# Kernel tuning notes

Hardware: AMD Instinct MI355X
Metric: run time of the kernel (lower is better)

The kernel has to match this reference:

```python
import jax, jax.numpy as jnp
import numpy as np

L = 3
NUM_NODES = 4000
NUM_RELS = 200
V = 20
EMB = 128
HID = 128
OUT = 100
N = 50000
E = 800000
B = 32
DECAY = 0.03


def setup_inputs() -> dict:
    key = jax.random.key(0)
    ks = jax.random.split(key, 20)
    s = 0.05  # weight scale
    inp = {
        'node_emb': jax.random.normal(ks[0], (NUM_NODES, EMB), jnp.float32) * s,
        'rel_emb': jax.random.normal(ks[1], (NUM_RELS, EMB), jnp.float32) * s,
        'lin_w': jax.random.normal(ks[2], (HID, EMB), jnp.float32) * s,  # torch Linear weight [out,in]
        'lin_b': jnp.zeros((HID,), jnp.float32),
        'alpha_w': jax.random.normal(ks[3], (L, NUM_NODES, NUM_NODES), jnp.float32) * 0.01,
        'alpha_b': jnp.zeros((L, NUM_NODES), jnp.float32),
        'beta_w': jax.random.normal(ks[4], (L, NUM_NODES), jnp.float32) * 0.01,
        'beta_b': jnp.zeros((L,), jnp.float32),
        'wr_w': jax.random.normal(ks[5], (L, HID), jnp.float32) * s,
        'wr_b': jnp.zeros((L,), jnp.float32),
        'conv_w': jax.random.normal(ks[6], (L, HID, HID), jnp.float32) * s,
        'conv_b': jnp.zeros((L, HID), jnp.float32),
        'mlp_w': jax.random.normal(ks[7], (OUT, 2 * HID), jnp.float32) * s,
        'mlp_b': jnp.zeros((OUT,), jnp.float32),
        'visit_node': jax.random.uniform(ks[8], (B, V, NUM_NODES), jnp.float32),
        'ehr_nodes': jax.random.uniform(ks[9], (B, NUM_NODES), jnp.float32),
        'node_ids': jax.random.randint(ks[10], (N,), 0, NUM_NODES, jnp.int32),
        'rel_ids': jax.random.randint(ks[11], (E,), 0, NUM_RELS, jnp.int32),
        'edge_index': jax.random.randint(ks[12], (2, E), 0, N, jnp.int32),
        'batch': jnp.sort(jax.random.randint(ks[13], (N,), 0, B, jnp.int32)),
    }
    return inp


def reference(node_emb, rel_emb, lin_w, lin_b, alpha_w, alpha_b, beta_w, beta_b,
              wr_w, wr_b, conv_w, conv_b, mlp_w, mlp_b, visit_node, ehr_nodes,
              node_ids, rel_ids, edge_index, batch):
    # initial node / edge features
    x = node_emb[node_ids] @ lin_w.T + lin_b                # [N, HID]
    edge_attr = rel_emb[rel_ids] @ lin_w.T + lin_b          # [E, HID]

    # temporal decay per visit: lambda_j = exp(decay*(V - j)), shape [1, V, 1]
    j = jnp.arange(V, dtype=jnp.float32)
    lam = jnp.exp(DECAY * (V - j))[None, :, None]

    src = edge_index[0]
    dst = edge_index[1]
    xj_nid = node_ids[src]                                  # [E]
    xj_bat = batch[src]                                     # [E]

    for l in range(L):
        # alpha: softmax over the visit axis (dim=1)
        alpha = jax.nn.softmax(
            jnp.einsum('bvn,mn->bvm', visit_node, alpha_w[l]) + alpha_b[l], axis=1)
        beta = jnp.tanh(
            jnp.einsum('bvn,n->bv', visit_node, beta_w[l])[:, :, None] + beta_b[l]) * lam
        attn = jnp.sum(alpha * beta, axis=1)                # [B, NUM_NODES]
        e_attn = attn[xj_bat, xj_nid][:, None]              # [E, 1]

        # BiAttentionGNNConv message + add-aggregate
        w_rel = edge_attr @ wr_w[l][:, None] + wr_b[l]      # [E, 1]
        msg = jax.nn.relu(x[src] * e_attn + w_rel * edge_attr)
        agg = jax.ops.segment_sum(msg, dst, num_segments=N)
        out = agg + x                                       # eps = 0 -> (1+eps)=1
        x = out @ conv_w[l].T + conv_b[l]                   # conv.nn Linear
        x = jax.nn.relu(x)                                  # outer F.relu (dropout inactive in eval)

    # global mean pool over graphs
    cnt = jax.ops.segment_sum(jnp.ones((N,), x.dtype), batch, num_segments=B)
    x_graph = jax.ops.segment_sum(x, batch, num_segments=B) / jnp.maximum(cnt, 1.0)[:, None]

    # patient node embedding branch
    x_node = (ehr_nodes @ node_emb) / jnp.sum(ehr_nodes, axis=1, keepdims=True)
    x_node = x_node @ lin_w.T + lin_b                       # [B, HID]

    logits = jnp.concatenate([x_graph, x_node], axis=1) @ mlp_w.T + mlp_b
    return logits
```

## Files before the change

kernel.cpp:

```cpp
#include <hip/hip_runtime.h>
#include <hip/hip_bf16.h>
#include <stdint.h>

#define LL      3
#define NNODES  4000
#define NRELS   200
#define VV      20
#define EMB     128
#define HIDD    128
#define OUTD    100
#define WS_N    50000
#define WS_E    800000
#define BV      32
#define DECAYF  0.03f
#define AK      4032
#define ZSTRIDE ((long)LL*640*4000)
#define SCAN_NB 196
#define NPP     391

typedef __bf16 bf16x8 __attribute__((ext_vector_type(8)));
typedef __bf16 bf16x4 __attribute__((ext_vector_type(4)));
typedef __bf16 bf16x2 __attribute__((ext_vector_type(2)));
typedef float  f32x4  __attribute__((ext_vector_type(4)));

__device__ __forceinline__ void glds16(const __bf16* g, __bf16* l) {
    __builtin_amdgcn_global_load_lds((const __attribute__((address_space(1))) void*)g,
                                     (__attribute__((address_space(3))) void*)l, 16, 0, 0);
}

__global__ __launch_bounds__(256) void k_cvt2(const float* __restrict__ visit,
                                              const float* __restrict__ alpha_w,
                                              const float* __restrict__ beta_w,
                                              const float* __restrict__ beta_b,
                                              __bf16* __restrict__ visit_bf,
                                              __bf16* __restrict__ alpha_bf,
                                              float* __restrict__ betab) {
    long bid = blockIdx.x;
    const bool isv = bid < BV*VV;
    const float* ip; __bf16* op;
    if (isv) { ip = visit + bid*4000; op = visit_bf + bid*AK; }
    else     { long r = bid - BV*VV; ip = alpha_w + r*4000; op = alpha_bf + r*AK; }
    int t = threadIdx.x;
    float p0 = 0.f, p1 = 0.f, p2 = 0.f;
    if (t < 250) {
        const float4* p4 = (const float4*)ip + t*4;
        float4 f0 = p4[0], f1 = p4[1], f2 = p4[2], f3 = p4[3];
        bf16x8 h0, h1;
        h0[0]=(__bf16)f0.x; h0[1]=(__bf16)f0.y; h0[2]=(__bf16)f0.z; h0[3]=(__bf16)f0.w;
        h0[4]=(__bf16)f1.x; h0[5]=(__bf16)f1.y; h0[6]=(__bf16)f1.z; h0[7]=(__bf16)f1.w;
        h1[0]=(__bf16)f2.x; h1[1]=(__bf16)f2.y; h1[2]=(__bf16)f2.z; h1[3]=(__bf16)f2.w;
        h1[4]=(__bf16)f3.x; h1[5]=(__bf16)f3.y; h1[6]=(__bf16)f3.z; h1[7]=(__bf16)f3.w;
        ((bf16x8*)op)[t*2]   = h0;
        ((bf16x8*)op)[t*2+1] = h1;
        if (isv) {
            #pragma unroll
            for (int l = 0; l < LL; l++) {
                const float4* bw = (const float4*)(beta_w + (long)l*4000) + t*4;
                float4 b0 = bw[0], b1 = bw[1], b2 = bw[2], b3 = bw[3];
                float s = f0.x*b0.x + f0.y*b0.y + f0.z*b0.z + f0.w*b0.w
                        + f1.x*b1.x + f1.y*b1.y + f1.z*b1.z + f1.w*b1.w
                        + f2.x*b2.x + f2.y*b2.y + f2.z*b2.z + f2.w*b2.w
                        + f3.x*b3.x + f3.y*b3.y + f3.z*b3.z + f3.w*b3.w;
                if (l == 0) p0 = s; else if (l == 1) p1 = s; else p2 = s;
            }
        }
    } else if (t < 254) {
        bf16x8 zz;
        #pragma unroll
        for (int j = 0; j < 8; j++) zz[j] = (__bf16)0.f;
        ((bf16x8*)op)[500 + (t - 250)] = zz;
    }
    if (isv) {
        __shared__ float r0[256], r1[256], r2[256];
        r0[t] = p0; r1[t] = p1; r2[t] = p2;
        __syncthreads();
        for (int o = 128; o > 0; o >>= 1) {
            if (t < o) { r0[t] += r0[t+o]; r1[t] += r1[t+o]; r2[t] += r2[t+o]; }
            __syncthreads();
        }
        if (t == 0) {
            int v = (int)(bid % VV);
            float lam = __expf(DECAYF * (float)(VV - v));
            betab[0*BV*VV + bid] = tanhf(r0[0] + beta_b[0]) * lam;
            betab[1*BV*VV + bid] = tanhf(r1[0] + beta_b[1]) * lam;
            betab[2*BV*VV + bid] = tanhf(r2[0] + beta_b[2]) * lam;
        }
    }
}

__global__ __launch_bounds__(256)
void gemm_alpha(const __bf16* __restrict__ visit_bf, const __bf16* __restrict__ alpha_bf,
                __bf16* __restrict__ zpart)
{
    __shared__ __bf16 Ah[128*64];
    __shared__ __bf16 Bh[128*64];

    const int id   = blockIdx.x;
    const int xcd  = id & 7;
    const int slot = id >> 3;
    const int mi   = slot % 5;
    const int gix  = slot / 5;
    const int g    = xcd * 48 + gix;
    const int ni   = g & 31;
    const int lkh  = g >> 5;
    const int l    = lkh >> 2;
    const int kh   = lkh & 3;

    const __bf16* Ag = visit_bf;
    const __bf16* Bg = alpha_bf + (long)l * NNODES * AK;
    __bf16*       Cg = zpart + (long)kh * ZSTRIDE + (long)l * 640 * 4000;
    const int m0 = mi * 128;
    const int n0 = ni * 128;
    const int k0 = kh * 1024;
    const int k1 = (kh == 3) ? AK : (k0 + 1024);

    const int tid = threadIdx.x;
    const int wv  = tid >> 6;
    const int ln  = tid & 63;
    const int srow = ln >> 3;
    const int gsl  = (ln & 7) ^ srow;

    const __bf16* aA = Ag + (long)(m0 + wv*8 + srow) * AK + gsl*8;
    const __bf16* bB[4];
    #pragma unroll
    for (int t = 0; t < 4; t++) {
        int br = n0 + wv*8 + srow + t*32;
        if (br > NNODES-1) br = NNODES-1;
        bB[t] = Bg + (long)br * AK + gsl*8;
    }

    const int wm = (wv & 1) * 64;
    const int wn = (wv >> 1) * 64;
    const int lr = ln & 15;
    const int kq = ln >> 4;
    const int sw0 = lr & 7;

    f32x4 acc[4][4];
    #pragma unroll
    for (int i = 0; i < 4; i++)
        #pragma unroll
        for (int j = 0; j < 4; j++)
            acc[i][j] = (f32x4){0.f, 0.f, 0.f, 0.f};

    for (int kb = k0; kb < k1; kb += 64) {
        #pragma unroll
        for (int t = 0; t < 4; t++) {
            glds16(aA + (long)t*32*AK + kb, &Ah[(t*4 + wv) * 512]);
            glds16(bB[t] + kb,              &Bh[(t*4 + wv) * 512]);
        }
        __syncthreads();
        #pragma unroll
        for (int ks = 0; ks < 2; ks++) {
            const int sg = ((ks*4 + kq) ^ sw0) * 8;
            bf16x8 af[4], bfr[4];
            #pragma unroll
            for (int i = 0; i < 4; i++) {
                af[i]  = *(const bf16x8*)&Ah[(wm + i*16 + lr)*64 + sg];
                bfr[i] = *(const bf16x8*)&Bh[(wn + i*16 + lr)*64 + sg];
            }
            #pragma unroll
            for (int i = 0; i < 4; i++)
                #pragma unroll
                for (int j = 0; j < 4; j++)
                    acc[i][j] = __builtin_amdgcn_mfma_f32_16x16x32_bf16(af[i], bfr[j], acc[i][j], 0, 0, 0);
        }
        __syncthreads();
    }

    #pragma unroll
    for (int i = 0; i < 4; i++) {
        const int row_b = m0 + wm + i*16 + kq*4;
        #pragma unroll
        for (int j = 0; j < 4; j++) {
            const int col = n0 + wn + j*16 + lr;
            if (col < NNODES) {
                #pragma unroll
                for (int r = 0; r < 4; r++)
                    Cg[(long)(row_b + r)*4000 + col] = (__bf16)acc[i][j][r];
            }
        }
    }
}

#define BM 128
#define BN 128
#define BKG 32
#define LSTR 40

template<int SPLIT>
__device__ __forceinline__ void stage_tile(const float* __restrict__ G, int rows, int Kdim,
                                           int r0, int kb, int k1, __bf16* Sh, __bf16* Sl, int tid)
{
    const int sr  = tid >> 1;
    const int skc = (tid & 1) * 16;
    const int gr  = r0 + sr;
    const int gk  = kb + skc;
    float va[16];
    if (gr < rows && gk + 16 <= k1) {
        const float4* p4 = (const float4*)(G + (long)gr * Kdim + gk);
        #pragma unroll
        for (int q = 0; q < 4; q++) {
            float4 f = p4[q];
            va[4*q+0] = f.x; va[4*q+1] = f.y; va[4*q+2] = f.z; va[4*q+3] = f.w;
        }
    } else {
        #pragma unroll
        for (int j = 0; j < 16; j++) {
            int kk = gk + j;
            va[j] = (gr < rows && kk < k1) ? G[(long)gr * Kdim + kk] : 0.0f;
        }
    }
    bf16x8 h[2], lo[2];
    #pragma unroll
    for (int half = 0; half < 2; half++) {
        #pragma unroll
        for (int j = 0; j < 8; j++) {
            float v = va[half*8 + j];
            __bf16 hi = (__bf16)v;
            h[half][j]  = hi;
            lo[half][j] = (__bf16)(v - (float)hi);
        }
    }
    *(bf16x8*)&Sh[sr*LSTR + skc]     = h[0];
    *(bf16x8*)&Sh[sr*LSTR + skc + 8] = h[1];
    if (SPLIT) {
        *(bf16x8*)&Sl[sr*LSTR + skc]     = lo[0];
        *(bf16x8*)&Sl[sr*LSTR + skc + 8] = lo[1];
    }
}

template<int SPLIT, int RELU, int BIAS, int WRITEB>
__global__ __launch_bounds__(256)
void gemm_bt(const float* __restrict__ Ag, const float* __restrict__ Bg,
             float* __restrict__ Cg, const float* __restrict__ bias,
             __bf16* __restrict__ Xb, int M, int N, int K)
{
    __shared__ __bf16 Ah[BM*LSTR];
    __shared__ __bf16 Bh[BN*LSTR];
    __shared__ __bf16 Alo[SPLIT ? BM*LSTR : 1];
    __shared__ __bf16 Blo[SPLIT ? BN*LSTR : 1];

    const int tid = threadIdx.x;
    const int m0 = blockIdx.x * BM;
    const int n0 = blockIdx.y * BN;

    const int wave = tid >> 6;
    const int lane = tid & 63;
    const int wm = (wave & 1) * 64;
    const int wn = (wave >> 1) * 64;
    const int lr = lane & 15;
    const int kq = lane >> 4;

    f32x4 acc[4][4];
    #pragma unroll
    for (int i = 0; i < 4; i++)
        #pragma unroll
        for (int j = 0; j < 4; j++)
            acc[i][j] = (f32x4){0.f, 0.f, 0.f, 0.f};

    for (int kb = 0; kb < K; kb += BKG) {
        stage_tile<SPLIT>(Ag, M, K, m0, kb, K, Ah, Alo, tid);
        stage_tile<SPLIT>(Bg, N, K, n0, kb, K, Bh, Blo, tid);
        __syncthreads();

        bf16x8 af[4], bfr[4];
        #pragma unroll
        for (int i = 0; i < 4; i++) {
            af[i]  = *(const bf16x8*)&Ah[(wm + i*16 + lr)*LSTR + kq*8];
            bfr[i] = *(const bf16x8*)&Bh[(wn + i*16 + lr)*LSTR + kq*8];
        }
        #pragma unroll
        for (int i = 0; i < 4; i++)
            #pragma unroll
            for (int j = 0; j < 4; j++)
                acc[i][j] = __builtin_amdgcn_mfma_f32_16x16x32_bf16(af[i], bfr[j], acc[i][j], 0, 0, 0);

        if (SPLIT) {
            bf16x8 al[4], bl[4];
            #pragma unroll
            for (int i = 0; i < 4; i++) {
                al[i] = *(const bf16x8*)&Alo[(wm + i*16 + lr)*LSTR + kq*8];
                bl[i] = *(const bf16x8*)&Blo[(wn + i*16 + lr)*LSTR + kq*8];
            }
            #pragma unroll
            for (int i = 0; i < 4; i++)
                #pragma unroll
                for (int j = 0; j < 4; j++) {
                    acc[i][j] = __builtin_amdgcn_mfma_f32_16x16x32_bf16(af[i], bl[j], acc[i][j], 0, 0, 0);
                    acc[i][j] = __builtin_amdgcn_mfma_f32_16x16x32_bf16(al[i], bfr[j], acc[i][j], 0, 0, 0);
                }
        }
        __syncthreads();
    }

    #pragma unroll
    for (int i = 0; i < 4; i++) {
        const int row_b = m0 + wm + i*16 + kq*4;
        #pragma unroll
        for (int j = 0; j < 4; j++) {
            const int col = n0 + wn + j*16 + lr;
            if (col < N) {
                #pragma unroll
                for (int r = 0; r < 4; r++) {
                    const int row = row_b + r;
                    if (row < M) {
                        float v = acc[i][j][r];
                        if (BIAS) v += bias[col];
                        if (RELU) v = fmaxf(v, 0.0f);
                        Cg[(long)row*N + col] = v;
                        if (WRITEB) Xb[(long)row*N + col] = (__bf16)v;
                    }
                }
            }
        }
    }
}

__global__ void k_count(const int* __restrict__ dst, int* __restrict__ deg) {
    int e = blockIdx.x*256 + threadIdx.x;
    if (e < WS_E) atomicAdd(&deg[dst[e]], 1);
}

__global__ __launch_bounds__(256) void k_scan1(const int* __restrict__ deg, int* __restrict__ bsum) {
    __shared__ int red[256];
    int t = threadIdx.x;
    int i = blockIdx.x*256 + t;
    red[t] = (i < WS_N) ? deg[i] : 0;
    __syncthreads();
    for (int o = 128; o > 0; o >>= 1) {
        if (t < o) red[t] += red[t + o];
        __syncthreads();
    }
    if (t == 0) bsum[blockIdx.x] = red[0];
}

__global__ __launch_bounds__(256) void k_scan3(const int* __restrict__ deg, const int* __restrict__ bsum,
                                               int* __restrict__ offs, int* __restrict__ cursor) {
    __shared__ int sb[256];
    __shared__ int s[256];
    int t = threadIdx.x;
    int bv = (t < SCAN_NB) ? bsum[t] : 0;
    sb[t] = bv;
    __syncthreads();
    for (int o = 1; o < 256; o <<= 1) {
        int add = (t >= o) ? sb[t - o] : 0;
        __syncthreads();
        sb[t] += add;
        __syncthreads();
    }
    int base = (blockIdx.x == 0) ? 0 : sb[blockIdx.x - 1];

    int i = blockIdx.x*256 + t;
    int v = (i < WS_N) ? deg[i] : 0;
    s[t] = v;
    __syncthreads();
    for (int o = 1; o < 256; o <<= 1) {
        int add = (t >= o) ? s[t - o] : 0;
        __syncthreads();
        s[t] += add;
        __syncthreads();
    }
    if (i < WS_N) {
        int e = base + s[t] - v;
        offs[i] = e;
        cursor[i] = e;
    }
    if (blockIdx.x == 0 && t == 0) offs[WS_N] = WS_E;
}

__global__ void k_fill(const int* __restrict__ dst, const int* __restrict__ src,
                       const int* __restrict__ rel, int* __restrict__ cursor,
                       int2* __restrict__ sr) {
    int e = blockIdx.x*256 + threadIdx.x;
    if (e < WS_E) {
        int d = dst[e];
        int p = atomicAdd(&cursor[d], 1);
        sr[p] = make_int2(src[e], rel[e]);
    }
}

__global__ __launch_bounds__(128) void k_relfused(const float* __restrict__ rel_emb,
                                                  const float* __restrict__ lin_w,
                                                  const float* __restrict__ lin_b,
                                                  const float* __restrict__ wr_w,
                                                  const float* __restrict__ wr_b,
                                                  __bf16* __restrict__ relmsg) {
    int r = blockIdx.x;
    int o = threadIdx.x;
    __shared__ float row[128];
    __shared__ float red[128];
    row[o] = rel_emb[(long)r*EMB + o];
    __syncthreads();
    float wv = lin_b[o];
    #pragma unroll 4
    for (int k = 0; k < EMB; k++) wv += row[k] * lin_w[(long)o*EMB + k];
    #pragma unroll
    for (int l = 0; l < LL; l++) {
        red[o] = wv * wr_w[l*HIDD + o];
        __syncthreads();
        for (int s2 = 64; s2 > 0; s2 >>= 1) {
            if (o < s2) red[o] += red[o + s2];
            __syncthreads();
        }
        float wrel = red[0] + wr_b[l];
        __syncthreads();
        relmsg[((long)l*NRELS + r)*HIDD + o] = (__bf16)(wrel * wv);
    }
}

__global__ void k_xinit(const float* __restrict__ Wnode, const int* __restrict__ nid,
                        const int* __restrict__ batch, const float* __restrict__ attn,
                        float* __restrict__ x, __bf16* __restrict__ xb, float* __restrict__ an) {
    int t = blockIdx.x*256 + threadIdx.x;
    if (t >= WS_N*32) return;
    int i = t >> 5;
    int d = t & 31;
    int n = nid[i];
    float4 v = ((const float4*)Wnode)[n*32 + d];
    ((float4*)x)[i*32 + d] = v;
    bf16x4 b;
    b[0] = (__bf16)v.x; b[1] = (__bf16)v.y; b[2] = (__bf16)v.z; b[3] = (__bf16)v.w;
    ((bf16x4*)xb)[i*32 + d] = b;
    if (d < LL) an[(long)d*WS_N + i] = attn[((long)d*BV + batch[i]) * NNODES + n];
}

__global__ __launch_bounds__(256) void k_attnpool(const __bf16* __restrict__ zpart,
                                                  const float* __restrict__ beta, float* __restrict__ attn) {
    int m = blockIdx.x*256 + threadIdx.x;
    int b = blockIdx.y;
    int l = blockIdx.z;
    if (m >= NNODES) return;
    const __bf16* zp = zpart + ((long)l*640 + b*VV) * 4000 + m;
    const float* bet = beta + (l*BV + b) * VV;
    float zv[VV];
    float mx = -1e30f;
    #pragma unroll
    for (int v = 0; v < VV; v++) {
        long o = (long)v * 4000;
        float s = (float)zp[o] + (float)zp[ZSTRIDE + o] + (float)zp[2*ZSTRIDE + o] + (float)zp[3*ZSTRIDE + o];
        zv[v] = s;
        mx = fmaxf(mx, s);
    }
    float s = 0.f, ws = 0.f;
    #pragma unroll
    for (int v = 0; v < VV; v++) {
        float e = __expf(zv[v] - mx);
        s += e;
        ws += e * bet[v];
    }
    attn[((long)l*BV + b) * NNODES + m] = ws / s;
}

__global__ __launch_bounds__(256) void k_agg(const float* __restrict__ x, const __bf16* __restrict__ xb,
                                             const float* __restrict__ an,
                                             const __bf16* __restrict__ relmsg_l, const int* __restrict__ offs,
                                             const int2* __restrict__ sr,
                                             float* __restrict__ outb) {
    int node = blockIdx.x*4 + (threadIdx.x >> 6);
    if (node >= WS_N) return;
    int lane = threadIdx.x & 63;
    int half = lane >> 5;
    int lh   = lane & 31;
    int e0 = offs[node], e1 = offs[node + 1];
    const bf16x4* xb4 = (const bf16x4*)xb;
    const bf16x4* rm4 = (const bf16x4*)relmsg_l;
    float a0 = 0.f, a1 = 0.f, a2 = 0.f, a3 = 0.f;
    int e = e0;
    for (; e + 8 <= e1; e += 8) {
        int2 pe[4];
        #pragma unroll
        for (int q = 0; q < 4; q++) pe[q] = sr[e + 2*q + half];
        float aq[4]; bf16x4 gv[4], mv[4];
        #pragma unroll
        for (int q = 0; q < 4; q++) aq[q] = an[pe[q].x];
        #pragma unroll
        for (int q = 0; q < 4; q++) gv[q] = xb4[pe[q].x*32 + lh];
        #pragma unroll
        for (int q = 0; q < 4; q++) mv[q] = rm4[pe[q].y*32 + lh];
        #pragma unroll
        for (int q = 0; q < 4; q++) {
            a0 += fmaxf((float)gv[q][0]*aq[q] + (float)mv[q][0], 0.f);
            a1 += fmaxf((float)gv[q][1]*aq[q] + (float)mv[q][1], 0.f);
            a2 += fmaxf((float)gv[q][2]*aq[q] + (float)mv[q][2], 0.f);
            a3 += fmaxf((float)gv[q][3]*aq[q] + (float)mv[q][3], 0.f);
        }
    }
    for (; e < e1; e += 2) {
        int ei = e + half;
        bool vld = ei < e1;
        int2 pe = sr[vld ? ei : e];
        float aa = vld ? an[pe.x] : 0.f;
        bf16x4 ga = xb4[pe.x*32 + lh];
        bf16x4 va = rm4[pe.y*32 + lh];
        float vm = vld ? 1.f : 0.f;
        a0 += vm * fmaxf((float)ga[0]*aa + (float)va[0], 0.f);
        a1 += vm * fmaxf((float)ga[1]*aa + (float)va[1], 0.f);
        a2 += vm * fmaxf((float)ga[2]*aa + (float)va[2], 0.f);
        a3 += vm * fmaxf((float)ga[3]*aa + (float)va[3], 0.f);
    }
    a0 += __shfl_xor(a0, 32);
    a1 += __shfl_xor(a1, 32);
    a2 += __shfl_xor(a2, 32);
    a3 += __shfl_xor(a3, 32);
    if (half == 0) {
        float4 xo = ((const float4*)x)[node*32 + lh];
        float4 r;
        r.x = a0 + xo.x; r.y = a1 + xo.y; r.z = a2 + xo.z; r.w = a3 + xo.w;
        ((float4*)outb)[node*32 + lh] = r;
    }
}

__global__ __launch_bounds__(256) void k_pool(const float* __restrict__ x,
                                              const int* __restrict__ batch,
                                              const float* __restrict__ ehr,
                                              const float* __restrict__ node_emb,
                                              float* __restrict__ xgsum,
                                              float* __restrict__ xnsum,
                                              float* __restrict__ esum) {
    if (blockIdx.x < NPP) {
        int r0 = blockIdx.x * 128;
        int d = threadIdx.x & 127;
        int rofs = threadIdx.x >> 7;
        int r1 = min(r0 + 128, WS_N);
        float acc = 0.f;
        int curb = -1;
        for (int i = r0 + rofs; i < r1; i += 2) {
            int b = batch[i];
            if (b != curb) {
                if (curb >= 0) atomicAdd(&xgsum[curb*HIDD + d], acc);
                acc = 0.f; curb = b;
            }
            acc += x[(long)i*HIDD + d];
        }
        if (curb >= 0) atomicAdd(&xgsum[curb*HIDD + d], acc);
    } else {
        int id = blockIdx.x - NPP;
        int b = id >> 4;
        int c = id & 15;
        int d = threadIdx.x;
        int n0 = c * (NNODES/16), n1 = n0 + (NNODES/16);
        __shared__ float red[256];
        if (d < 128) {
            float acc = 0.f;
            for (int n = n0; n < n1; n++)
                acc += ehr[b*NNODES + n] * node_emb[(long)n*HIDD + d];
            atomicAdd(&xnsum[b*HIDD + d], acc);
        }
        float s = 0.f;
        for (int n = n0 + d; n < n1; n += 256) s += ehr[b*NNODES + n];
        red[d] = s; __syncthreads();
        for (int o = 128; o > 0; o >>= 1) {
            if (d < o) red[d] += red[d + o];
            __syncthreads();
        }
        if (d == 0) atomicAdd(&esum[b], red[0]);
    }
}

__global__ __launch_bounds__(128) void k_head(const float* __restrict__ xgsum,
                                              const float* __restrict__ xnsum,
                                              const float* __restrict__ esum,
                                              const int* __restrict__ batch,
                                              const float* __restrict__ lin_w, const float* __restrict__ lin_b,
                                              const float* __restrict__ mlp_w, const float* __restrict__ mlp_b,
                                              float* __restrict__ out) {
    int b = blockIdx.x;
    int d = threadIdx.x;
    int lo = 0, hi = WS_N;
    while (lo < hi) { int mid = (lo + hi) >> 1; if (batch[mid] < b) lo = mid + 1; else hi = mid; }
    int s0 = lo;
    lo = 0; hi = WS_N;
    while (lo < hi) { int mid = (lo + hi) >> 1; if (batch[mid] < b + 1) lo = mid + 1; else hi = mid; }
    int cnt = max(lo - s0, 1);
    __shared__ float t1[128];
    __shared__ float cat[2*HIDD];
    t1[d]  = xnsum[b*HIDD + d] / esum[b];
    cat[d] = xgsum[b*HIDD + d] / (float)cnt;
    __syncthreads();
    float o2 = lin_b[d];
    for (int k2 = 0; k2 < HIDD; k2++) o2 += t1[k2] * lin_w[d*HIDD + k2];
    cat[HIDD + d] = o2;
    __syncthreads();
    if (d < OUTD) {
        float a = mlp_b[d];
        for (int j = 0; j < 2*HIDD; j++) a += cat[j] * mlp_w[d*2*HIDD + j];
        out[b*OUTD + d] = a;
    }
}

extern "C" void kernel_launch(void* const* d_in, const int* in_sizes, int n_in,
                              void* d_out, int out_size, void* d_ws, size_t ws_size,
                              hipStream_t stream)
{
    const float* node_emb = (const float*)d_in[0];
    const float* rel_emb  = (const float*)d_in[1];
    const float* lin_w    = (const float*)d_in[2];
    const float* lin_b    = (const float*)d_in[3];
    const float* alpha_w  = (const float*)d_in[4];
    const float* beta_w   = (const float*)d_in[6];
    const float* beta_b   = (const float*)d_in[7];
    const float* wr_w     = (const float*)d_in[8];
    const float* wr_b     = (const float*)d_in[9];
    const float* conv_w   = (const float*)d_in[10];
    const float* conv_b   = (const float*)d_in[11];
    const float* mlp_w    = (const float*)d_in[12];
    const float* mlp_b    = (const float*)d_in[13];
    const float* visit    = (const float*)d_in[14];
    const float* ehr      = (const float*)d_in[15];
    const int* node_ids   = (const int*)d_in[16];
    const int* rel_ids    = (const int*)d_in[17];
    const int* ei         = (const int*)d_in[18];
    const int* batch      = (const int*)d_in[19];
    const int* esrc = ei;
    const int* edst = ei + WS_E;
    float* out = (float*)d_out;

    char* p = (char*)d_ws;
    auto take = [&](size_t bytes) -> char* {
        char* q = p;
        p += (bytes + 255) & ~(size_t)255;
        return q;
    };
    __bf16* zpart    = (__bf16*)take((size_t)4*ZSTRIDE*2);
    __bf16* visit_bf = (__bf16*)take((size_t)(BV*VV)*AK*2);
    char*   big      = take((size_t)LL*NNODES*AK*2);
    float* betab  = (float*)take((size_t)LL*BV*VV*4);
    float* xgsum  = (float*)take((size_t)BV*HIDD*4);
    float* xnsum  = (float*)take((size_t)BV*HIDD*4);
    float* esum   = (float*)take((size_t)BV*4);
    int* deg      = (int*)take((size_t)WS_N*4);
    size_t zero_bytes = (size_t)((char*)(deg + WS_N) - (char*)xgsum);
    int* offs     = (int*)take((size_t)(WS_N+1)*4);
    int* cursor   = (int*)take((size_t)WS_N*4);
    int* bsum     = (int*)take((size_t)SCAN_NB*4);
    if ((size_t)(p - (char*)d_ws) > ws_size) return;

    __bf16* alpha_bf = (__bf16*)big;
    char* q = big;
    auto carve = [&](size_t bytes) -> char* {
        char* r = q;
        q += (bytes + 255) & ~(size_t)255;
        return r;
    };
    float*  x      = (float*)carve((size_t)WS_N*HIDD*4);
    __bf16* xb     = (__bf16*)carve((size_t)WS_N*HIDD*2);
    int2*   sr     = (int2*)carve((size_t)WS_E*8);
    float*  attn   = (float*)carve((size_t)LL*BV*NNODES*4);
    float*  attnnd = (float*)carve((size_t)LL*WS_N*4);
    float*  Wnode  = (float*)carve((size_t)NNODES*HIDD*4);
    __bf16* relmsg = (__bf16*)carve((size_t)LL*NRELS*HIDD*2);
    float*  aggbuf = (float*)zpart;

    (void)hipMemsetAsync(xgsum, 0, zero_bytes, stream);

    k_cvt2<<<dim3(BV*VV + LL*NNODES), 256, 0, stream>>>(visit, alpha_w, beta_w, beta_b,
                                                        visit_bf, alpha_bf, betab);
    gemm_alpha<<<dim3(1920), 256, 0, stream>>>(visit_bf, alpha_bf, zpart);
    k_attnpool<<<dim3((NNODES+255)/256, BV, LL), 256, 0, stream>>>(zpart, betab, attn);

    k_count<<<dim3((WS_E+255)/256), 256, 0, stream>>>(edst, deg);
    k_scan1<<<dim3(SCAN_NB), 256, 0, stream>>>(deg, bsum);
    k_scan3<<<dim3(SCAN_NB), 256, 0, stream>>>(deg, bsum, offs, cursor);
    k_fill<<<dim3((WS_E+255)/256), 256, 0, stream>>>(edst, esrc, rel_ids, cursor, sr);

    gemm_bt<1,0,1,0><<<dim3((NNODES+BM-1)/BM, 1, 1), 256, 0, stream>>>(
        node_emb, lin_w, Wnode, lin_b, nullptr, NNODES, HIDD, HIDD);
    k_relfused<<<dim3(NRELS), 128, 0, stream>>>(rel_emb, lin_w, lin_b, wr_w, wr_b, relmsg);
    k_xinit<<<dim3((WS_N*32+255)/256), 256, 0, stream>>>(Wnode, node_ids, batch, attn, x, xb, attnnd);

    for (int l = 0; l < LL; l++) {
        k_agg<<<dim3((WS_N+3)/4), 256, 0, stream>>>(
            x, xb, attnnd + (size_t)l*WS_N, relmsg + (size_t)l*NRELS*HIDD, offs, sr, aggbuf);
        gemm_bt<1,1,1,1><<<dim3((WS_N+BM-1)/BM, 1, 1), 256, 0, stream>>>(
            aggbuf, conv_w + (size_t)l*HIDD*HIDD, x, conv_b + (size_t)l*HIDD, xb,
            WS_N, HIDD, HIDD);
    }

    k_pool<<<dim3(NPP + 16*BV), 256, 0, stream>>>(x, batch, ehr, node_emb, xgsum, xnsum, esum);
    k_head<<<BV, 128, 0, stream>>>(xgsum, xnsum, esum, batch, lin_w, lin_b, mlp_w, mlp_b, out);
}
```

Before: 820.1 us.

## Pack edge src/rel into 32-bit, widen agg loads, fuse degree count

Edge records are packed into one uint32 (16-bit src, 16-bit rel) instead of int2, which halves CSR edge traffic in the fill and aggregation kernels. k_agg now uses 16 lanes with bf16x8 loads per edge and processes 4 edges in parallel per wavefront, reduced with two shuffles. The degree-count kernel is folded into the conversion kernel's grid to save a launch, and the last layer's GEMM skips writing the bf16 copy of x. Packing src into 16 bits relies on node indices staying below 65536 (N=50000 fits), and the grid-size change drops the node bound check, which is only safe because N is divisible by 4.

```diff
diff --git a/kernel.cpp b/kernel.cpp
--- a/kernel.cpp
+++ b/kernel.cpp
@@ -17,6 +17,8 @@
 #define ZSTRIDE ((long)LL*640*4000)
 #define SCAN_NB 196
 #define NPP     391
+#define CVT_NB  (BV*VV + LL*NNODES)
+#define CNT_NB  ((WS_E+255)/256)
 
 typedef __bf16 bf16x8 __attribute__((ext_vector_type(8)));
 typedef __bf16 bf16x4 __attribute__((ext_vector_type(4)));
@@ -34,13 +36,20 @@
                                               const float* __restrict__ beta_b,
                                               __bf16* __restrict__ visit_bf,
                                               __bf16* __restrict__ alpha_bf,
-                                              float* __restrict__ betab) {
+                                              float* __restrict__ betab,
+                                              const int* __restrict__ edst,
+                                              int* __restrict__ deg) {
     long bid = blockIdx.x;
+    int t = threadIdx.x;
+    if (bid >= CVT_NB) {
+        int e = (int)(bid - CVT_NB)*256 + t;
+        if (e < WS_E) atomicAdd(&deg[edst[e]], 1);
+        return;
+    }
     const bool isv = bid < BV*VV;
     const float* ip; __bf16* op;
     if (isv) { ip = visit + bid*4000; op = visit_bf + bid*AK; }
     else     { long r = bid - BV*VV; ip = alpha_w + r*4000; op = alpha_bf + r*AK; }
-    int t = threadIdx.x;
     float p0 = 0.f, p1 = 0.f, p2 = 0.f;
     if (t < 250) {
         const float4* p4 = (const float4*)ip + t*4;
@@ -316,11 +325,6 @@
     }
 }
 
-__global__ void k_count(const int* __restrict__ dst, int* __restrict__ deg) {
-    int e = blockIdx.x*256 + threadIdx.x;
-    if (e < WS_E) atomicAdd(&deg[dst[e]], 1);
-}
-
 __global__ __launch_bounds__(256) void k_scan1(const int* __restrict__ deg, int* __restrict__ bsum) {
     __shared__ int red[256];
     int t = threadIdx.x;
@@ -370,12 +374,12 @@
 
 __global__ void k_fill(const int* __restrict__ dst, const int* __restrict__ src,
                        const int* __restrict__ rel, int* __restrict__ cursor,
-                       int2* __restrict__ sr) {
+                       uint32_t* __restrict__ sr) {
     int e = blockIdx.x*256 + threadIdx.x;
     if (e < WS_E) {
         int d = dst[e];
         int p = atomicAdd(&cursor[d], 1);
-        sr[p] = make_int2(src[e], rel[e]);
+        sr[p] = (uint32_t)src[e] | ((uint32_t)rel[e] << 16);
     }
 }
 
@@ -454,59 +458,65 @@
 __global__ __launch_bounds__(256) void k_agg(const float* __restrict__ x, const __bf16* __restrict__ xb,
                                              const float* __restrict__ an,
                                              const __bf16* __restrict__ relmsg_l, const int* __restrict__ offs,
-                                             const int2* __restrict__ sr,
+                                             const uint32_t* __restrict__ sr,
                                              float* __restrict__ outb) {
     int node = blockIdx.x*4 + (threadIdx.x >> 6);
-    if (node >= WS_N) return;
     int lane = threadIdx.x & 63;
-    int half = lane >> 5;
-    int lh   = lane & 31;
+    int eh = lane >> 4;
+    int lh = lane & 15;
     int e0 = offs[node], e1 = offs[node + 1];
-    const bf16x4* xb4 = (const bf16x4*)xb;
-    const bf16x4* rm4 = (const bf16x4*)relmsg_l;
-    float a0 = 0.f, a1 = 0.f, a2 = 0.f, a3 = 0.f;
+    const bf16x8* xb8 = (const bf16x8*)xb;
+    const bf16x8* rm8 = (const bf16x8*)relmsg_l;
+    float acc[8];
+    #pragma unroll
+    for (int d = 0; d < 8; d++) acc[d] = 0.f;
     int e = e0;
     for (; e + 8 <= e1; e += 8) {
-        int2 pe[4];
-        #pragma unroll
-        for (int q = 0; q < 4; q++) pe[q] = sr[e + 2*q + half];
-        float aq[4]; bf16x4 gv[4], mv[4];
-        #pragma unroll
-        for (int q = 0; q < 4; q++) aq[q] = an[pe[q].x];
-        #pragma unroll
-        for (int q = 0; q < 4; q++) gv[q] = xb4[pe[q].x*32 + lh];
-        #pragma unroll
-        for (int q = 0; q < 4; q++) mv[q] = rm4[pe[q].y*32 + lh];
-        #pragma unroll
-        for (int q = 0; q < 4; q++) {
-            a0 += fmaxf((float)gv[q][0]*aq[q] + (float)mv[q][0], 0.f);
-            a1 += fmaxf((float)gv[q][1]*aq[q] + (float)mv[q][1], 0.f);
-            a2 += fmaxf((float)gv[q][2]*aq[q] + (float)mv[q][2], 0.f);
-            a3 += fmaxf((float)gv[q][3]*aq[q] + (float)mv[q][3], 0.f);
-        }
-    }
-    for (; e < e1; e += 2) {
-        int ei = e + half;
-        bool vld = ei < e1;
-        int2 pe = sr[vld ? ei : e];
-        float aa = vld ? an[pe.x] : 0.f;
-        bf16x4 ga = xb4[pe.x*32 + lh];
-        bf16x4 va = rm4[pe.y*32 + lh];
-        float vm = vld ? 1.f : 0.f;
-        a0 += vm * fmaxf((float)ga[0]*aa + (float)va[0], 0.f);
-        a1 += vm * fmaxf((float)ga[1]*aa + (float)va[1], 0.f);
-        a2 += vm * fmaxf((float)ga[2]*aa + (float)va[2], 0.f);
-        a3 += vm * fmaxf((float)ga[3]*aa + (float)va[3], 0.f);
-    }
-    a0 += __shfl_xor(a0, 32);
-    a1 += __shfl_xor(a1, 32);
-    a2 += __shfl_xor(a2, 32);
-    a3 += __shfl_xor(a3, 32);
-    if (half == 0) {
-        float4 xo = ((const float4*)x)[node*32 + lh];
-        float4 r;
-        r.x = a0 + xo.x; r.y = a1 + xo.y; r.z = a2 + xo.z; r.w = a3 + xo.w;
-        ((float4*)outb)[node*32 + lh] = r;
+        uint32_t p0 = sr[e + eh], p1 = sr[e + 4 + eh];
+        int s0 = p0 & 0xFFFF, r0 = p0 >> 16;
+        int s1 = p1 & 0xFFFF, r1 = p1 >> 16;
+        float a0 = an[s0], a1 = an[s1];
+        bf16x8 g0 = xb8[s0*16 + lh], g1 = xb8[s1*16 + lh];
+        bf16x8 m0 = rm8[r0*16 + lh], m1 = rm8[r1*16 + lh];
+        #pragma unroll
+        for (int d = 0; d < 8; d++) {
+            acc[d] += fmaxf((float)g0[d]*a0 + (float)m0[d], 0.f);
+            acc[d] += fmaxf((float)g1[d]*a1 + (float)m1[d], 0.f);
+        }
+    }
+    for (; e + 4 <= e1; e += 4) {
+        uint32_t p = sr[e + eh];
+        int s = p & 0xFFFF, r = p >> 16;
+        float a = an[s];
+        bf16x8 g = xb8[s*16 + lh];
+        bf16x8 m = rm8[r*16 + lh];
+        #pragma unroll
+        for (int d = 0; d < 8; d++)
+            acc[d] += fmaxf((float)g[d]*a + (float)m[d], 0.f);
+    }
+    if (e + eh < e1) {
+        uint32_t p = sr[e + eh];
+        int s = p & 0xFFFF, r = p >> 16;
+        float a = an[s];
+        bf16x8 g = xb8[s*16 + lh];
+        bf16x8 m = rm8[r*16 + lh];
+        #pragma unroll
+        for (int d = 0; d < 8; d++)
+            acc[d] += fmaxf((float)g[d]*a + (float)m[d], 0.f);
+    }
+    #pragma unroll
+    for (int d = 0; d < 8; d++) {
+        acc[d] += __shfl_xor(acc[d], 16);
+        acc[d] += __shfl_xor(acc[d], 32);
+    }
+    if (eh == 0) {
+        float4 x0 = ((const float4*)x)[node*32 + lh*2];
+        float4 x1 = ((const float4*)x)[node*32 + lh*2 + 1];
+        float4 o0, o1;
+        o0.x = acc[0] + x0.x; o0.y = acc[1] + x0.y; o0.z = acc[2] + x0.z; o0.w = acc[3] + x0.w;
+        o1.x = acc[4] + x1.x; o1.y = acc[5] + x1.y; o1.z = acc[6] + x1.z; o1.w = acc[7] + x1.w;
+        ((float4*)outb)[node*32 + lh*2]     = o0;
+        ((float4*)outb)[node*32 + lh*2 + 1] = o1;
     }
 }
 
@@ -642,23 +652,22 @@
         q += (bytes + 255) & ~(size_t)255;
         return r;
     };
-    float*  x      = (float*)carve((size_t)WS_N*HIDD*4);
-    __bf16* xb     = (__bf16*)carve((size_t)WS_N*HIDD*2);
-    int2*   sr     = (int2*)carve((size_t)WS_E*8);
-    float*  attn   = (float*)carve((size_t)LL*BV*NNODES*4);
-    float*  attnnd = (float*)carve((size_t)LL*WS_N*4);
-    float*  Wnode  = (float*)carve((size_t)NNODES*HIDD*4);
-    __bf16* relmsg = (__bf16*)carve((size_t)LL*NRELS*HIDD*2);
-    float*  aggbuf = (float*)zpart;
+    float*    x      = (float*)carve((size_t)WS_N*HIDD*4);
+    __bf16*   xb     = (__bf16*)carve((size_t)WS_N*HIDD*2);
+    uint32_t* sr     = (uint32_t*)carve((size_t)WS_E*4);
+    float*    attn   = (float*)carve((size_t)LL*BV*NNODES*4);
+    float*    attnnd = (float*)carve((size_t)LL*WS_N*4);
+    float*    Wnode  = (float*)carve((size_t)NNODES*HIDD*4);
+    __bf16*   relmsg = (__bf16*)carve((size_t)LL*NRELS*HIDD*2);
+    float*    aggbuf = (float*)zpart;
 
     (void)hipMemsetAsync(xgsum, 0, zero_bytes, stream);
 
-    k_cvt2<<<dim3(BV*VV + LL*NNODES), 256, 0, stream>>>(visit, alpha_w, beta_w, beta_b,
-                                                        visit_bf, alpha_bf, betab);
+    k_cvt2<<<dim3(CVT_NB + CNT_NB), 256, 0, stream>>>(visit, alpha_w, beta_w, beta_b,
+                                                      visit_bf, alpha_bf, betab, edst, deg);
     gemm_alpha<<<dim3(1920), 256, 0, stream>>>(visit_bf, alpha_bf, zpart);
     k_attnpool<<<dim3((NNODES+255)/256, BV, LL), 256, 0, stream>>>(zpart, betab, attn);
 
-    k_count<<<dim3((WS_E+255)/256), 256, 0, stream>>>(edst, deg);
     k_scan1<<<dim3(SCAN_NB), 256, 0, stream>>>(deg, bsum);
     k_scan3<<<dim3(SCAN_NB), 256, 0, stream>>>(deg, bsum, offs, cursor);
     k_fill<<<dim3((WS_E+255)/256), 256, 0, stream>>>(edst, esrc, rel_ids, cursor, sr);
@@ -669,11 +678,16 @@
     k_xinit<<<dim3((WS_N*32+255)/256), 256, 0, stream>>>(Wnode, node_ids, batch, attn, x, xb, attnnd);
 
     for (int l = 0; l < LL; l++) {
-        k_agg<<<dim3((WS_N+3)/4), 256, 0, stream>>>(
+        k_agg<<<dim3(WS_N/4), 256, 0, stream>>>(
             x, xb, attnnd + (size_t)l*WS_N, relmsg + (size_t)l*NRELS*HIDD, offs, sr, aggbuf);
-        gemm_bt<1,1,1,1><<<dim3((WS_N+BM-1)/BM, 1, 1), 256, 0, stream>>>(
-            aggbuf, conv_w + (size_t)l*HIDD*HIDD, x, conv_b + (size_t)l*HIDD, xb,
-            WS_N, HIDD, HIDD);
+        if (l < LL-1)
+            gemm_bt<1,1,1,1><<<dim3((WS_N+BM-1)/BM, 1, 1), 256, 0, stream>>>(
+                aggbuf, conv_w + (size_t)l*HIDD*HIDD, x, conv_b + (size_t)l*HIDD, xb,
+                WS_N, HIDD, HIDD);
+        else
+            gemm_bt<1,1,1,0><<<dim3((WS_N+BM-1)/BM, 1, 1), 256, 0, stream>>>(
+                aggbuf, conv_w + (size_t)l*HIDD*HIDD, x, conv_b + (size_t)l*HIDD, nullptr,
+                WS_N, HIDD, HIDD);
     }
 
     k_pool<<<dim3(NPP + 16*BV), 256, 0, stream>>>(x, batch, ehr, node_emb, xgsum, xnsum, esum);
```

Result: faster. 771.5 us (-5.9%).
